# Kernel optimization log

Measured on AMD Instinct MI355X. Metric: run time of the kernel, lower is better.

Reference implementation:

```python
import jax, jax.numpy as jnp
import numpy as np

C = 64
CQK = C // 8  # query/key channels = 8


def setup_inputs() -> dict:
    key = jax.random.key(0)
    ks = jax.random.split(key, 7)
    B, D, H, W = 1, 16, 32, 32
    x = jax.random.normal(ks[0], (B, C, D, H, W), dtype=jnp.float32)
    # 1x1x1 Conv3d weights collapse to [out_ch, in_ch] matrices; std=0.01 per nn.init.normal_
    wq = 0.01 * jax.random.normal(ks[1], (CQK, C), dtype=jnp.float32)
    bq = jnp.zeros((CQK,), dtype=jnp.float32)
    wk = 0.01 * jax.random.normal(ks[2], (CQK, C), dtype=jnp.float32)
    bk = jnp.zeros((CQK,), dtype=jnp.float32)
    wv = 0.01 * jax.random.normal(ks[3], (C, C), dtype=jnp.float32)
    bv = jnp.zeros((C,), dtype=jnp.float32)
    gamma = jnp.zeros((1,), dtype=jnp.float32)  # nn.Parameter(torch.zeros(1))
    return {"x": x, "wq": wq, "bq": bq, "wk": wk, "bk": bk, "wv": wv, "bv": bv, "gamma": gamma}


def reference(x, wq, bq, wk, bk, wv, bv, gamma):
    B, Cc, D, H, W = x.shape
    N = D * H * W
    xf = x.reshape(B, Cc, N)  # [B, C, N]
    # 1x1x1 convs == per-position linear projections
    q = jnp.einsum('oc,bcn->bon', wq, xf) + bq[None, :, None]   # [B, CQK, N]
    k = jnp.einsum('oc,bcn->bon', wk, xf) + bk[None, :, None]   # [B, CQK, N]
    v = jnp.einsum('oc,bcn->bon', wv, xf) + bv[None, :, None]   # [B, C, N]
    # attention[b, i, j] = softmax_j( q[:, :, i] . k[:, :, j] )  -> [B, N, N]
    scores = jnp.einsum('bon,bom->bnm', q, k)
    attn = jax.nn.softmax(scores, axis=-1)
    # out[b, c, i] = sum_j v[b, c, j] * attn[b, i, j]
    out = jnp.einsum('bcm,bnm->bcn', v, attn).reshape(B, Cc, D, H, W)
    return x + gamma * out
```

## Files before the change

### kernel.cpp

```cpp
#include <hip/hip_runtime.h>

#define NPOS 16384
#define KSPLIT 8
#define KEYS_PER_BLK (NPOS / KSPLIT)
#define CHUNK 512
#define LOG2E 1.4426950408889634f

typedef short bf16x8 __attribute__((ext_vector_type(8)));
typedef unsigned short u16x8 __attribute__((ext_vector_type(8)));
typedef float floatx16 __attribute__((ext_vector_type(16)));
typedef float floatx2 __attribute__((ext_vector_type(2)));

static __device__ __forceinline__ unsigned short f2bf(float f) {
    return (unsigned short)(__builtin_bit_cast(unsigned int, f) >> 16);
}
static __device__ __forceinline__ float bf2f(unsigned short h) {
    return __builtin_bit_cast(float, (unsigned int)h << 16);
}

#if __has_builtin(__builtin_amdgcn_exp2f)
static __device__ __forceinline__ float exp2_fast(float x) {
    return __builtin_amdgcn_exp2f(x);
}
#else
static __device__ __forceinline__ float exp2_fast(float x) {
    float r;
    asm("v_exp_f32 %0, %1" : "=v"(r) : "v"(x));
    return r;
}
#endif

static __device__ __forceinline__ unsigned int pk_bf16(float e_even, float e_odd) {
    return __builtin_amdgcn_perm(__builtin_bit_cast(unsigned int, e_odd),
                                 __builtin_bit_cast(unsigned int, e_even),
                                 0x07060302u);
}

static __device__ __forceinline__ int sigma(int n) {
    const int w12 = n & 12;
    return (w12 == 4 || w12 == 8) ? (n ^ 12) : n;
}

__global__ __launch_bounds__(256) void proj_kernel(
    const float* __restrict__ x,
    const float* __restrict__ wq, const float* __restrict__ bq,
    const float* __restrict__ wk, const float* __restrict__ bk,
    const float* __restrict__ wv, const float* __restrict__ bv,
    unsigned short* __restrict__ qb16, unsigned short* __restrict__ kb16,
    unsigned short* __restrict__ vbg16)
{
    const int t = threadIdx.x;
    const int n = blockIdx.x * 256 + t;
    const int g = blockIdx.y;

    const float* w;
    const float* b;
    if (g == 0)      { w = wq; b = bq; }
    else if (g == 1) { w = wk; b = bk; }
    else             { w = wv + (g - 2) * 8 * 64; b = bv + (g - 2) * 8; }

    float acc[8];
#pragma unroll
    for (int oo = 0; oo < 8; ++oo) acc[oo] = b[oo];
#pragma unroll 16
    for (int c = 0; c < 64; ++c) {
        const float xv = x[c * NPOS + n];
#pragma unroll
        for (int oo = 0; oo < 8; ++oo)
            acc[oo] = fmaf(w[oo * 64 + c], xv, acc[oo]);
    }

    if (g == 0) {
        u16x8 qp;
#pragma unroll
        for (int j = 0; j < 8; ++j) qp[j] = f2bf(acc[j] * LOG2E);
        ((uint4*)qb16)[n] = __builtin_bit_cast(uint4, qp);
    } else if (g == 1) {
        u16x8 kp;
#pragma unroll
        for (int j = 0; j < 8; ++j) kp[j] = f2bf(acc[j]);
        ((uint4*)kb16)[n] = __builtin_bit_cast(uint4, kp);
    } else {
        const int o0 = (g - 2) * 8;
        const int np = sigma(n);
        const size_t base = (size_t)(np >> 3) * 512 + (np & 7);
#pragma unroll
        for (int oo = 0; oo < 8; ++oo)
            vbg16[base + (size_t)(o0 + oo) * 8] = f2bf(acc[oo]);
    }
}

__global__ __launch_bounds__(256, 4) void attn_kernel(
    const uint4* __restrict__ qb4,
    const uint4* __restrict__ kb4,
    const uint4* __restrict__ vbg4,
    unsigned short* __restrict__ nump,
    float* __restrict__ denp)
{
    __shared__ __align__(16) char smem[16896];
    uint4* k_lds = (uint4*)smem;

    const int t     = threadIdx.x;
    const int wave  = t >> 6;
    const int lane  = t & 63;
    const int m     = lane & 31;
    const int half  = lane >> 5;
    const int qpair = wave >> 1;
    const int khalf = wave & 1;

    const int qblk = blockIdx.x >> 3;
    const int kq   = blockIdx.x & 7;
    const int i0   = qblk * 128;
    const int jb   = kq * KEYS_PER_BLK;
    const int qt0  = (i0 >> 5) + qpair * 2;

    const uint4 zero4 = make_uint4(0, 0, 0, 0);
    const uint4 qLo4 = (half == 0) ? qb4[i0 + qpair * 64 + m]      : zero4;
    const uint4 qHi4 = (half == 0) ? qb4[i0 + qpair * 64 + 32 + m] : zero4;
    const bf16x8 bqLo = __builtin_bit_cast(bf16x8, qLo4);
    const bf16x8 bqHi = __builtin_bit_cast(bf16x8, qHi4);

    floatx16 accLoA = {}, accLoB = {};
    floatx16 accHiA = {}, accHiB = {};
    floatx2  dLo = {0.f, 0.f}, dHi = {0.f, 0.f};

#pragma unroll 1
    for (int c4 = 0; c4 < 4; ++c4) {
        const int j0 = jb + c4 * CHUNK;
        __syncthreads();
        k_lds[t]       = kb4[j0 + t];
        k_lds[256 + t] = kb4[j0 + 256 + t];
        __syncthreads();

        const int kwb = khalf * 256;
#pragma unroll 1
        for (int st = 0; st < 8; ++st) {
            const int kb_ = kwb + st * 32;
            const bf16x8 ak = __builtin_bit_cast(bf16x8, k_lds[kb_ + m]);
            const floatx16 sLo = __builtin_amdgcn_mfma_f32_32x32x16_bf16(
                ak, bqLo, (floatx16){}, 0, 0, 0);
            const floatx16 sHi = __builtin_amdgcn_mfma_f32_32x32x16_bf16(
                ak, bqHi, (floatx16){}, 0, 0, 0);

            const int g8t = (j0 + kb_) >> 3;
            bf16x8 vf0[2], vf1[2];
#pragma unroll
            for (int f = 0; f < 2; ++f) {
                const int g8 = g8t + f * 2 + half;
                vf0[f] = __builtin_bit_cast(bf16x8, vbg4[(size_t)g8 * 64 + m]);
                vf1[f] = __builtin_bit_cast(bf16x8,
                                            vbg4[(size_t)g8 * 64 + 32 + m]);
            }

            {
                float e[16];
#pragma unroll
                for (int r = 0; r < 16; ++r) e[r] = exp2_fast(sLo[r]);
#pragma unroll
                for (int p = 0; p < 8; ++p)
                    dLo += (floatx2){e[2 * p], e[2 * p + 1]};
                unsigned int P[8];
#pragma unroll
                for (int p = 0; p < 8; ++p)
                    P[p] = pk_bf16(e[2 * p], e[2 * p + 1]);
#pragma unroll
                for (int f = 0; f < 2; ++f) {
                    uint4 afu;
                    afu.x = P[4 * f + 0];
                    afu.y = P[4 * f + 1];
                    afu.z = P[4 * f + 2];
                    afu.w = P[4 * f + 3];
                    const bf16x8 af = __builtin_bit_cast(bf16x8, afu);
                    accLoA = __builtin_amdgcn_mfma_f32_32x32x16_bf16(
                        af, vf0[f], accLoA, 0, 0, 0);
                    accLoB = __builtin_amdgcn_mfma_f32_32x32x16_bf16(
                        af, vf1[f], accLoB, 0, 0, 0);
                }
            }
            {
                float e[16];
#pragma unroll
                for (int r = 0; r < 16; ++r) e[r] = exp2_fast(sHi[r]);
#pragma unroll
                for (int p = 0; p < 8; ++p)
                    dHi += (floatx2){e[2 * p], e[2 * p + 1]};
                unsigned int P[8];
#pragma unroll
                for (int p = 0; p < 8; ++p)
                    P[p] = pk_bf16(e[2 * p], e[2 * p + 1]);
#pragma unroll
                for (int f = 0; f < 2; ++f) {
                    uint4 afu;
                    afu.x = P[4 * f + 0];
                    afu.y = P[4 * f + 1];
                    afu.z = P[4 * f + 2];
                    afu.w = P[4 * f + 3];
                    const bf16x8 af = __builtin_bit_cast(bf16x8, afu);
                    accHiA = __builtin_amdgcn_mfma_f32_32x32x16_bf16(
                        af, vf0[f], accHiA, 0, 0, 0);
                    accHiB = __builtin_amdgcn_mfma_f32_32x32x16_bf16(
                        af, vf1[f], accHiB, 0, 0, 0);
                }
            }
        }
    }

    const float dlLo = dLo[0] + dLo[1];
    const float dwLo = dlLo + __shfl_xor(dlLo, 32);
    const float dlHi = dHi[0] + dHi[1];
    const float dwHi = dlHi + __shfl_xor(dlHi, 32);

    __syncthreads();
    float*          xden = (float*)smem;
    unsigned short* xacc = (unsigned short*)(smem + 512);
    if (khalf == 1) {
        if (half == 0) {
            xden[(qpair * 2 + 0) * 32 + m] = dwLo;
            xden[(qpair * 2 + 1) * 32 + m] = dwHi;
        }
#pragma unroll
        for (int tile = 0; tile < 2; ++tile) {
            const floatx16* aA = tile ? &accHiA : &accLoA;
            const floatx16* aB = tile ? &accHiB : &accLoB;
            u16x8 a0, a1, a2, a3;
#pragma unroll
            for (int j = 0; j < 8; ++j) {
                a0[j] = f2bf((*aA)[j]);
                a1[j] = f2bf((*aA)[8 + j]);
                a2[j] = f2bf((*aB)[j]);
                a3[j] = f2bf((*aB)[8 + j]);
            }
            uint4* dst = (uint4*)(xacc + ((qpair * 2 + tile) * 64 + lane) * 32);
            dst[0] = __builtin_bit_cast(uint4, a0);
            dst[1] = __builtin_bit_cast(uint4, a1);
            dst[2] = __builtin_bit_cast(uint4, a2);
            dst[3] = __builtin_bit_cast(uint4, a3);
        }
    }
    __syncthreads();
    if (khalf == 0) {
#pragma unroll
        for (int tile = 0; tile < 2; ++tile) {
            const floatx16* aA = tile ? &accHiA : &accLoA;
            const floatx16* aB = tile ? &accHiB : &accLoB;
            const uint4* src =
                (const uint4*)(xacc + ((qpair * 2 + tile) * 64 + lane) * 32);
            const u16x8 b0 = __builtin_bit_cast(u16x8, src[0]);
            const u16x8 b1 = __builtin_bit_cast(u16x8, src[1]);
            const u16x8 b2 = __builtin_bit_cast(u16x8, src[2]);
            const u16x8 b3 = __builtin_bit_cast(u16x8, src[3]);
            u16x8 o0, o1, o2, o3;
#pragma unroll
            for (int j = 0; j < 8; ++j) {
                o0[j] = f2bf((*aA)[j]      + bf2f(b0[j]));
                o1[j] = f2bf((*aA)[8 + j]  + bf2f(b1[j]));
                o2[j] = f2bf((*aB)[j]      + bf2f(b2[j]));
                o3[j] = f2bf((*aB)[8 + j]  + bf2f(b3[j]));
            }
            const size_t base =
                (((size_t)kq * 512 + qt0 + tile) * 64 + lane) * 32;
            uint4* gdst = (uint4*)(nump + base);
            gdst[0] = __builtin_bit_cast(uint4, o0);
            gdst[1] = __builtin_bit_cast(uint4, o1);
            gdst[2] = __builtin_bit_cast(uint4, o2);
            gdst[3] = __builtin_bit_cast(uint4, o3);
        }
        if (half == 0) {
            denp[(size_t)kq * NPOS + (qt0 + 0) * 32 + m] =
                dwLo + xden[(qpair * 2 + 0) * 32 + m];
            denp[(size_t)kq * NPOS + (qt0 + 1) * 32 + m] =
                dwHi + xden[(qpair * 2 + 1) * 32 + m];
        }
    }
}

__global__ __launch_bounds__(256) void finalize_kernel(
    const float* __restrict__ x,
    const unsigned short* __restrict__ nump,
    const float* __restrict__ denp,
    const float* __restrict__ gamma,
    float* __restrict__ out)
{
    const int b    = blockIdx.x;
    const int t    = threadIdx.x;
    const int lane = t >> 2;
    const int u    = t & 3;
    const int n0   = b * 32;

    __shared__ float dsum[32];
    __shared__ float ot[32 * 66];
    if (t < 32) dsum[t] = 0.f;
    __syncthreads();
    atomicAdd(&dsum[t & 31], denp[(size_t)(t >> 5) * NPOS + n0 + (t & 31)]);

    float ns[8];
#pragma unroll
    for (int j = 0; j < 8; ++j) ns[j] = 0.f;
#pragma unroll
    for (int kq = 0; kq < 8; ++kq) {
        const size_t base =
            (((size_t)kq * 512 + b) * 64 + lane) * 32 + u * 8;
        const u16x8 h = __builtin_bit_cast(u16x8, *(const uint4*)(nump + base));
#pragma unroll
        for (int j = 0; j < 8; ++j) ns[j] += bf2f(h[j]);
    }

    const int clow = lane & 31;
    const int hf   = lane >> 5;
#pragma unroll
    for (int j = 0; j < 8; ++j) {
        const int off = u * 8 + j;
        const int r   = off & 15;
        const int row = (r & 3) + 8 * (r >> 2) + 4 * hf;
        const int c   = (off >> 4) * 32 + clow;
        ot[row * 66 + c] = ns[j];
    }
    __syncthreads();

    const float g  = gamma[0];
    const int   c2 = t >> 2;
    const int   nq = t & 3;
#pragma unroll
    for (int j = 0; j < 8; ++j) {
        const int row = nq * 8 + j;
        const size_t gi = (size_t)c2 * NPOS + n0 + row;
        out[gi] = fmaf(g, ot[row * 66 + c2] *
                              __builtin_amdgcn_rcpf(dsum[row]), x[gi]);
    }
}

extern "C" void kernel_launch(void* const* d_in, const int* in_sizes, int n_in,
                              void* d_out, int out_size, void* d_ws, size_t ws_size,
                              hipStream_t stream)
{
    (void)in_sizes; (void)n_in; (void)out_size; (void)ws_size;

    const float* x     = (const float*)d_in[0];
    const float* wq    = (const float*)d_in[1];
    const float* bq    = (const float*)d_in[2];
    const float* wk    = (const float*)d_in[3];
    const float* bk    = (const float*)d_in[4];
    const float* wv    = (const float*)d_in[5];
    const float* bv    = (const float*)d_in[6];
    const float* gamma = (const float*)d_in[7];
    float* out = (float*)d_out;

    char* ws = (char*)d_ws;
    unsigned short* qb16  = (unsigned short*)(ws);
    unsigned short* kb16  = (unsigned short*)(ws + 262144);
    unsigned short* vbg16 = (unsigned short*)(ws + 524288);
    unsigned short* nump  = (unsigned short*)(ws + 2621440);
    float*          denp  = (float*)(ws + 19398656);

    proj_kernel<<<dim3(NPOS / 256, 10), 256, 0, stream>>>(
        x, wq, bq, wk, bk, wv, bv, qb16, kb16, vbg16);
    attn_kernel<<<(NPOS / 128) * KSPLIT, 256, 0, stream>>>(
        (const uint4*)qb16, (const uint4*)kb16, (const uint4*)vbg16,
        nump, denp);
    finalize_kernel<<<512, 256, 0, stream>>>(x, nump, denp, gamma, out);
}
```

Before: 132.9 us.

## Fuse finalize into attention kernel via last-block atomic counter

Removes the separate finalize kernel. Each query block keeps an atomic counter, and the last of its 8 key-split blocks to finish reduces the partial numerators and denominators and writes the output. This saves one kernel launch and lets the finalize work overlap with other attention blocks, at the cost of threadfences, a memset launch, and a serialized tail in the last block. The score MFMAs are also moved next to their exp/pack consumers and merged into one loop, which may lower register pressure.

```diff
diff --git a/kernel.cpp b/kernel.cpp
--- a/kernel.cpp
+++ b/kernel.cpp
@@ -90,14 +90,31 @@
     }
 }
 
+static __device__ __forceinline__ void tile_post(
+    const floatx16& s, floatx2& dacc, unsigned int (&P)[8])
+{
+#pragma unroll
+    for (int p = 0; p < 8; ++p) {
+        const float e0 = exp2_fast(s[2 * p]);
+        const float e1 = exp2_fast(s[2 * p + 1]);
+        dacc += (floatx2){e0, e1};
+        P[p] = pk_bf16(e0, e1);
+    }
+}
+
 __global__ __launch_bounds__(256, 4) void attn_kernel(
     const uint4* __restrict__ qb4,
     const uint4* __restrict__ kb4,
     const uint4* __restrict__ vbg4,
     unsigned short* __restrict__ nump,
-    float* __restrict__ denp)
+    float* __restrict__ denp,
+    unsigned int* __restrict__ cnt,
+    const float* __restrict__ x,
+    const float* __restrict__ gamma,
+    float* __restrict__ out)
 {
     __shared__ __align__(16) char smem[16896];
+    __shared__ int sflag;
     uint4* k_lds = (uint4*)smem;
 
     const int t     = threadIdx.x;
@@ -137,10 +154,6 @@
         for (int st = 0; st < 8; ++st) {
             const int kb_ = kwb + st * 32;
             const bf16x8 ak = __builtin_bit_cast(bf16x8, k_lds[kb_ + m]);
-            const floatx16 sLo = __builtin_amdgcn_mfma_f32_32x32x16_bf16(
-                ak, bqLo, (floatx16){}, 0, 0, 0);
-            const floatx16 sHi = __builtin_amdgcn_mfma_f32_32x32x16_bf16(
-                ak, bqHi, (floatx16){}, 0, 0, 0);
 
             const int g8t = (j0 + kb_) >> 3;
             bf16x8 vf0[2], vf1[2];
@@ -153,16 +166,10 @@
             }
 
             {
-                float e[16];
-#pragma unroll
-                for (int r = 0; r < 16; ++r) e[r] = exp2_fast(sLo[r]);
-#pragma unroll
-                for (int p = 0; p < 8; ++p)
-                    dLo += (floatx2){e[2 * p], e[2 * p + 1]};
+                const floatx16 s = __builtin_amdgcn_mfma_f32_32x32x16_bf16(
+                    ak, bqLo, (floatx16){}, 0, 0, 0);
                 unsigned int P[8];
-#pragma unroll
-                for (int p = 0; p < 8; ++p)
-                    P[p] = pk_bf16(e[2 * p], e[2 * p + 1]);
+                tile_post(s, dLo, P);
 #pragma unroll
                 for (int f = 0; f < 2; ++f) {
                     uint4 afu;
@@ -178,16 +185,10 @@
                 }
             }
             {
-                float e[16];
-#pragma unroll
-                for (int r = 0; r < 16; ++r) e[r] = exp2_fast(sHi[r]);
-#pragma unroll
-                for (int p = 0; p < 8; ++p)
-                    dHi += (floatx2){e[2 * p], e[2 * p + 1]};
+                const floatx16 s = __builtin_amdgcn_mfma_f32_32x32x16_bf16(
+                    ak, bqHi, (floatx16){}, 0, 0, 0);
                 unsigned int P[8];
-#pragma unroll
-                for (int p = 0; p < 8; ++p)
-                    P[p] = pk_bf16(e[2 * p], e[2 * p + 1]);
+                tile_post(s, dHi, P);
 #pragma unroll
                 for (int f = 0; f < 2; ++f) {
                     uint4 afu;
@@ -272,60 +273,65 @@
                 dwHi + xden[(qpair * 2 + 1) * 32 + m];
         }
     }
-}
-
-__global__ __launch_bounds__(256) void finalize_kernel(
-    const float* __restrict__ x,
-    const unsigned short* __restrict__ nump,
-    const float* __restrict__ denp,
-    const float* __restrict__ gamma,
-    float* __restrict__ out)
-{
-    const int b    = blockIdx.x;
-    const int t    = threadIdx.x;
-    const int lane = t >> 2;
-    const int u    = t & 3;
-    const int n0   = b * 32;
-
-    __shared__ float dsum[32];
-    __shared__ float ot[32 * 66];
-    if (t < 32) dsum[t] = 0.f;
+
+    __threadfence();
     __syncthreads();
-    atomicAdd(&dsum[t & 31], denp[(size_t)(t >> 5) * NPOS + n0 + (t & 31)]);
-
-    float ns[8];
-#pragma unroll
-    for (int j = 0; j < 8; ++j) ns[j] = 0.f;
-#pragma unroll
-    for (int kq = 0; kq < 8; ++kq) {
-        const size_t base =
-            (((size_t)kq * 512 + b) * 64 + lane) * 32 + u * 8;
-        const u16x8 h = __builtin_bit_cast(u16x8, *(const uint4*)(nump + base));
-#pragma unroll
-        for (int j = 0; j < 8; ++j) ns[j] += bf2f(h[j]);
-    }
-
-    const int clow = lane & 31;
-    const int hf   = lane >> 5;
-#pragma unroll
-    for (int j = 0; j < 8; ++j) {
-        const int off = u * 8 + j;
-        const int r   = off & 15;
-        const int row = (r & 3) + 8 * (r >> 2) + 4 * hf;
-        const int c   = (off >> 4) * 32 + clow;
-        ot[row * 66 + c] = ns[j];
-    }
+    if (t == 0) sflag = (atomicAdd(&cnt[qblk], 1u) == 7u);
     __syncthreads();
-
-    const float g  = gamma[0];
-    const int   c2 = t >> 2;
-    const int   nq = t & 3;
-#pragma unroll
-    for (int j = 0; j < 8; ++j) {
-        const int row = nq * 8 + j;
-        const size_t gi = (size_t)c2 * NPOS + n0 + row;
-        out[gi] = fmaf(g, ot[row * 66 + c2] *
-                              __builtin_amdgcn_rcpf(dsum[row]), x[gi]);
+    if (!sflag) return;
+
+    __threadfence();
+    float* dsum = (float*)smem;
+    float* ot   = (float*)(smem + 128);
+    const float g    = gamma[0];
+    const int   lane4 = t >> 2;
+    const int   u     = t & 3;
+
+#pragma unroll 1
+    for (int tile = 0; tile < 4; ++tile) {
+        const int b4 = qblk * 4 + tile;
+        const int n0 = b4 * 32;
+
+        __syncthreads();
+        if (t < 32) dsum[t] = 0.f;
+        __syncthreads();
+        atomicAdd(&dsum[t & 31],
+                  denp[(size_t)(t >> 5) * NPOS + n0 + (t & 31)]);
+
+        float ns[8];
+#pragma unroll
+        for (int j = 0; j < 8; ++j) ns[j] = 0.f;
+#pragma unroll
+        for (int kk = 0; kk < 8; ++kk) {
+            const size_t base =
+                (((size_t)kk * 512 + b4) * 64 + lane4) * 32 + u * 8;
+            const u16x8 h =
+                __builtin_bit_cast(u16x8, *(const uint4*)(nump + base));
+#pragma unroll
+            for (int j = 0; j < 8; ++j) ns[j] += bf2f(h[j]);
+        }
+
+        const int clow = lane4 & 31;
+        const int hf   = lane4 >> 5;
+#pragma unroll
+        for (int j = 0; j < 8; ++j) {
+            const int off = u * 8 + j;
+            const int r   = off & 15;
+            const int row = (r & 3) + 8 * (r >> 2) + 4 * hf;
+            const int c   = (off >> 4) * 32 + clow;
+            ot[row * 66 + c] = ns[j];
+        }
+        __syncthreads();
+
+        const int c2 = t >> 2;
+        const int nq = t & 3;
+#pragma unroll
+        for (int j = 0; j < 8; ++j) {
+            const int row = nq * 8 + j;
+            const size_t gi = (size_t)c2 * NPOS + n0 + row;
+            out[gi] = fmaf(g, ot[row * 66 + c2] *
+                                  __builtin_amdgcn_rcpf(dsum[row]), x[gi]);
+        }
     }
 }
 
@@ -351,11 +357,13 @@
     unsigned short* vbg16 = (unsigned short*)(ws + 524288);
     unsigned short* nump  = (unsigned short*)(ws + 2621440);
     float*          denp  = (float*)(ws + 19398656);
+    unsigned int*   cnt   = (unsigned int*)(ws + 19922944);
+
+    hipMemsetAsync(cnt, 0, 128 * sizeof(unsigned int), stream);
 
     proj_kernel<<<dim3(NPOS / 256, 10), 256, 0, stream>>>(
         x, wq, bq, wk, bk, wv, bv, qb16, kb16, vbg16);
     attn_kernel<<<(NPOS / 128) * KSPLIT, 256, 0, stream>>>(
         (const uint4*)qb16, (const uint4*)kb16, (const uint4*)vbg16,
-        nump, denp);
-    finalize_kernel<<<512, 256, 0, stream>>>(x, nump, denp, gamma, out);
-}
+        nump, denp, cnt, x, gamma, out);
+}
```

After: 370.4 us. 2.79x slower.
